# Kernel optimization log

Hardware: AMD Instinct MI355X
Metric: run time of the kernel (lower is better)

Reference implementation:

```python
import jax, jax.numpy as jnp
import numpy as np

N_SAMPLES = 16384
L = 8000   # num pseudo labels
C = 8      # num cameras
D = 256    # feature dim
N = 512    # batch size
T = 0.05   # temperature
K = 50     # hard_neg_k
LW = 0.5   # inter-cam loss weight


def setup_inputs() -> dict:
    key = jax.random.key(0)
    k1, k2, k3, k4, k5 = jax.random.split(key, 5)
    feats = jax.random.normal(k1, (N, D), dtype=jnp.float32)
    indexes = jax.random.randint(k2, (N,), 0, N_SAMPLES)
    label_table = jax.random.randint(k3, (N_SAMPLES,), 0, L)
    cam_table = jax.random.randint(k4, (N_SAMPLES,), 0, C)
    centers = jax.random.normal(k5, (L * C, D), dtype=jnp.float32)
    centers = centers / jnp.linalg.norm(centers, axis=1, keepdims=True)
    return {"feats": feats, "indexes": indexes, "label_table": label_table,
            "cam_table": cam_table, "centers": centers}


def reference(feats, indexes, label_table, cam_table, centers):
    # F.normalize(feats, p=2, dim=1)
    feats = feats / jnp.linalg.norm(feats, axis=1, keepdims=True)
    labels = label_table[indexes]          # [n]
    cams = cam_table[indexes]              # [n]
    cen = jax.lax.stop_gradient(centers)   # centers are a non-grad buffer in torch

    all_sims = feats @ cen.T               # [n, P]  P = L*C, proxy(l,c) = l*C + c
    n, P = all_sims.shape
    sims_r = all_sims.reshape(n, L, C)     # [n, L, C]

    # ---- intra-camera loss: softmax over the L proxies sharing sample's camera ----
    idx_cam = jnp.broadcast_to(cams[:, None, None], (n, L, 1))
    sims_intra = jnp.take_along_axis(sims_r, idx_cam, axis=2)[..., 0]  # [n, L]
    logp_intra = jax.nn.log_softmax(sims_intra / T, axis=1)
    loss_intra_i = -jnp.take_along_axis(logp_intra, labels[:, None], axis=1)[:, 0]

    # ---- inter-camera loss: C positives (same label, all cams) + top-K hard negatives ----
    idx_lab = jnp.broadcast_to(labels[:, None, None], (n, 1, C))
    pos_sims = jnp.take_along_axis(sims_r, idx_lab, axis=1)[:, 0, :]   # [n, C]
    masked = jnp.where(jnp.arange(L)[None, :, None] == labels[:, None, None],
                       jnp.float32(-10000.0), sims_r).reshape(n, P)
    neg_sims, _ = jax.lax.top_k(masked, K)                             # [n, K]
    logits = jnp.concatenate([pos_sims, neg_sims], axis=1) / T         # [n, C+K]
    logp = jax.nn.log_softmax(logits, axis=1)
    loss_inter_i = -jnp.mean(logp[:, :C], axis=1)  # target = 1/C on the C positives

    # ---- per-camera mean, summed over cameras (matches the torch.unique loop) ----
    ones = jnp.ones((n,), feats.dtype)
    counts = jax.ops.segment_sum(ones, cams, num_segments=C)
    safe = jnp.maximum(counts, 1.0)
    s_intra = jax.ops.segment_sum(loss_intra_i, cams, num_segments=C)
    s_inter = jax.ops.segment_sum(loss_inter_i, cams, num_segments=C)
    loss_intra = jnp.sum(jnp.where(counts > 0, s_intra / safe, 0.0))
    loss_inter = LW * jnp.sum(jnp.where(counts > 0, s_inter / safe, 0.0))
    return jnp.stack([loss_intra, loss_inter])
```

## Files before the change

### kernel.cpp

```cpp
#include <hip/hip_runtime.h>
#include <stdint.h>

#define NS   512
#define DDIM 256
#define LL   8000
#define CC   8
#define PP   64000
#define KTOP 50
#define CAP  1024
#define NBLK 2000
#define K2C  28.853900817779268f

typedef float f32x4 __attribute__((ext_vector_type(4)));
typedef short bf16x8 __attribute__((ext_vector_type(8)));

__device__ __forceinline__ ushort f2bf(float x) {
    uint32_t b = __float_as_uint(x);
    b += 0x7fffu + ((b >> 16) & 1u);
    return (ushort)(b >> 16);
}
__device__ __forceinline__ float bf2f(ushort u) {
    return __uint_as_float(((uint32_t)u) << 16);
}

__global__ void k_norm_gather(const float* __restrict__ feats,
                              const int* __restrict__ indexes,
                              const int* __restrict__ ltab,
                              const int* __restrict__ ctab,
                              ushort* __restrict__ feats_b,
                              int* __restrict__ labels,
                              int* __restrict__ cams) {
    const int n = blockIdx.x;
    const int lane = threadIdx.x;
    f32x4 v = ((const f32x4*)(feats + (size_t)n * DDIM))[lane];
    float ss = v[0]*v[0] + v[1]*v[1] + v[2]*v[2] + v[3]*v[3];
#pragma unroll
    for (int off = 32; off > 0; off >>= 1) ss += __shfl_down(ss, off);
    float tot = __shfl(ss, 0);
    float sc = 1.0f / sqrtf(tot);
    ushort4 o;
    o.x = f2bf(v[0] * sc); o.y = f2bf(v[1] * sc);
    o.z = f2bf(v[2] * sc); o.w = f2bf(v[3] * sc);
    ((ushort4*)(feats_b + (size_t)n * DDIM))[lane] = o;
    if (lane == 0) {
        int idx = indexes[n];
        labels[n] = ltab[idx];
        cams[n] = ctab[idx];
    }
}

__global__ __launch_bounds__(256) void k_sigma(const ushort* __restrict__ fb,
                                               const float* __restrict__ B,
                                               float* __restrict__ sig_acc) {
    __shared__ float cf[DDIM];
    __shared__ float red[256];
    const int tid = threadIdx.x;
    const int p = blockIdx.x * 997 + 123;
    cf[tid] = bf2f(f2bf(B[(size_t)p * DDIM + tid]));
    __syncthreads();
    float s = 0.0f;
#pragma unroll
    for (int rr = 0; rr < 2; ++rr) {
        int r = tid * 2 + rr;
        const ushort* a = fb + (size_t)r * DDIM;
        float d = 0.0f;
        for (int k = 0; k < DDIM; k += 8) {
            bf16x8 av = *(const bf16x8*)(a + k);
#pragma unroll
            for (int j = 0; j < 8; ++j) d += bf2f((ushort)av[j]) * cf[k + j];
        }
        s += d * d;
    }
    red[tid] = s;
    __syncthreads();
    for (int off = 128; off > 0; off >>= 1) {
        if (tid < off) red[tid] += red[tid + off];
        __syncthreads();
    }
    if (tid == 0) atomicAdd(sig_acc, red[0]);
}

__global__ __launch_bounds__(256, 4)
void k_gemm_fused(const ushort* __restrict__ A, const float* __restrict__ B,
                  const int* __restrict__ labels, const int* __restrict__ cams,
                  const float* __restrict__ sig_acc,
                  float* __restrict__ partial, float* __restrict__ cand,
                  int* __restrict__ gcount, float* __restrict__ posbuf) {
    const int bx   = blockIdx.x;
    const int cBase = bx * 32;
    const int tid  = threadIdx.x;
    const int lane = tid & 63;
    const int w    = tid >> 6;
    const int lr   = lane & 15;
    const int lk   = lane >> 4;

    __shared__ ushort sB[32][264];
    __shared__ int   s_lab[NS];
    __shared__ int   s_cam[NS];
    __shared__ float s_intra[NS];

#pragma unroll
    for (int it = 0; it < 8; ++it) {
        int q   = tid + it * 256;
        int col = q >> 6;
        int k4  = q & 63;
        f32x4 a = *(const f32x4*)(B + (size_t)(cBase + col) * DDIM + k4 * 4);
        ushort4 o;
        o.x = f2bf(a[0]); o.y = f2bf(a[1]); o.z = f2bf(a[2]); o.w = f2bf(a[3]);
        *(ushort4*)(&sB[col][k4 * 4]) = o;
    }
    for (int r = tid; r < NS; r += 256) {
        s_lab[r] = labels[r];
        s_cam[r] = cams[r];
        s_intra[r] = 0.0f;
    }
    __syncthreads();

    const float tau = 2.9f * sqrtf(sig_acc[0] * (1.0f / 32768.0f));

    f32x4 zero = {0.f, 0.f, 0.f, 0.f};
    f32x4 acc[8][2];
#pragma unroll
    for (int m = 0; m < 8; ++m) { acc[m][0] = zero; acc[m][1] = zero; }

#pragma unroll
    for (int kb = 0; kb < 8; ++kb) {
        const int kpos = kb * 32 + lk * 8;
        bf16x8 b0 = *(const bf16x8*)(&sB[lr][kpos]);
        bf16x8 b1 = *(const bf16x8*)(&sB[16 + lr][kpos]);
#pragma unroll
        for (int m = 0; m < 8; ++m) {
            bf16x8 a = *(const bf16x8*)(A + (size_t)(w * 128 + m * 16 + lr) * DDIM + kpos);
            acc[m][0] = __builtin_amdgcn_mfma_f32_16x16x32_bf16(a, b0, acc[m][0], 0, 0, 0);
            acc[m][1] = __builtin_amdgcn_mfma_f32_16x16x32_bf16(a, b1, acc[m][1], 0, 0, 0);
        }
    }

#pragma unroll
    for (int m = 0; m < 8; ++m) {
#pragma unroll
        for (int j = 0; j < 4; ++j) {
            const int r   = w * 128 + m * 16 + lk * 4 + j;
            const int lab = s_lab[r];
            const int cm  = s_cam[r];
#pragma unroll
            for (int nn = 0; nn < 2; ++nn) {
                const int c_loc = nn * 16 + lr;
                const float v = acc[m][nn][j];
                if ((c_loc & 7) == cm)
                    atomicAdd(&s_intra[r], exp2f(v * K2C));
                const int g = (cBase + c_loc) >> 3;
                if (g == lab) {
                    posbuf[r * CC + (c_loc & 7)] = v;
                } else if (v > tau) {
                    int id = atomicAdd(&gcount[r], 1);
                    if (id < CAP) cand[(size_t)r * CAP + id] = v;
                }
            }
        }
    }
    __syncthreads();
    for (int r = tid; r < NS; r += 256)
        partial[(size_t)bx * NS + r] = s_intra[r];
}

__global__ __launch_bounds__(256) void k_fixup(const ushort* __restrict__ fb,
                                               const float* __restrict__ B,
                                               const int* __restrict__ labels,
                                               float* __restrict__ cand,
                                               int* __restrict__ gcount) {
    const int n = blockIdx.x;
    const int c0 = gcount[n];
    if (c0 >= KTOP && c0 <= CAP) return;

    const int tid = threadIdx.x;
    __shared__ float f[DDIM];
    __shared__ float s_lo, s_hi;
    __shared__ int   red[256];
    __shared__ int   s_done;
    __shared__ int   s_cnt;
    if (tid < DDIM) f[tid] = bf2f(fb[(size_t)n * DDIM + tid]);
    const int label = labels[n];
    if (tid == 0) { s_lo = -1.01f; s_hi = 1.01f; s_done = 0; }
    __syncthreads();

    for (int it = 0; it < 16 && !s_done; ++it) {
        float tm = 0.5f * (s_lo + s_hi);
        int cnt = 0;
        for (int p = tid; p < PP; p += 256) {
            if ((p >> 3) == label) continue;
            const float* col = B + (size_t)p * DDIM;
            float d = 0.0f;
            for (int k = 0; k < DDIM; ++k) d += f[k] * bf2f(f2bf(col[k]));
            cnt += (d > tm);
        }
        red[tid] = cnt;
        __syncthreads();
        for (int off = 128; off > 0; off >>= 1) {
            if (tid < off) red[tid] += red[tid + off];
            __syncthreads();
        }
        int tot = red[0];
        __syncthreads();
        if (tot >= KTOP && tot <= CAP) {
            if (tid == 0) s_cnt = 0;
            __syncthreads();
            for (int p = tid; p < PP; p += 256) {
                if ((p >> 3) == label) continue;
                const float* col = B + (size_t)p * DDIM;
                float d = 0.0f;
                for (int k = 0; k < DDIM; ++k) d += f[k] * bf2f(f2bf(col[k]));
                if (d > tm) {
                    int id = atomicAdd(&s_cnt, 1);
                    if (id < CAP) cand[(size_t)n * CAP + id] = d;
                }
            }
            __syncthreads();
            if (tid == 0) { gcount[n] = (s_cnt > CAP) ? CAP : s_cnt; s_done = 1; }
            __syncthreads();
        } else {
            if (tid == 0) { if (tot < KTOP) s_hi = tm; else s_lo = tm; }
            __syncthreads();
        }
    }
    if (s_done) return;
    if (tid == 0) s_cnt = 0;
    __syncthreads();
    float tl = s_lo;
    for (int p = tid; p < PP; p += 256) {
        if ((p >> 3) == label) continue;
        const float* col = B + (size_t)p * DDIM;
        float d = 0.0f;
        for (int k = 0; k < DDIM; ++k) d += f[k] * bf2f(f2bf(col[k]));
        if (d > tl) {
            int id = atomicAdd(&s_cnt, 1);
            if (id < CAP) cand[(size_t)n * CAP + id] = d;
        }
    }
    __syncthreads();
    if (tid == 0) gcount[n] = (s_cnt > CAP) ? CAP : s_cnt;
}

__global__ __launch_bounds__(256) void k_row(const float* __restrict__ partial,
                                             const float* __restrict__ cand,
                                             const int* __restrict__ gcount,
                                             const float* __restrict__ posbuf,
                                             const int* __restrict__ labels,
                                             const int* __restrict__ cams,
                                             float* __restrict__ li,
                                             float* __restrict__ le) {
    const int n = blockIdx.x;
    const int tid = threadIdx.x;
    __shared__ float red[256];
    __shared__ float spos[CC];
    __shared__ float scand[CAP];

    float s = 0.0f;
    for (int b = tid; b < NBLK; b += 256) s += partial[(size_t)b * NS + n];
    red[tid] = s;
    __syncthreads();
    for (int off = 128; off > 0; off >>= 1) {
        if (tid < off) red[tid] += red[tid + off];
        __syncthreads();
    }
    if (tid < CC) spos[tid] = posbuf[n * CC + tid];
    __syncthreads();
    if (tid == 0) li[n] = logf(red[0]) * 0.6931471805599453f / 0.6931471805599453f - 20.0f * spos[cams[n]];
    __syncthreads();

    int c = gcount[n];
    if (c > CAP) c = CAP;
    for (int i = tid; i < c; i += 256) scand[i] = cand[(size_t)n * CAP + i];
    __syncthreads();
    float sum = 0.0f;
    for (int i = tid; i < c; i += 256) {
        float v = scand[i];
        int rk = 0;
        for (int j = 0; j < c; ++j) {
            float u = scand[j];
            rk += (u > v) || (u == v && j < i);
        }
        if (rk < KTOP) sum += exp2f(v * K2C);
    }
    if (tid < CC) sum += exp2f(spos[tid] * K2C);
    red[tid] = sum;
    __syncthreads();
    for (int off = 128; off > 0; off >>= 1) {
        if (tid < off) red[tid] += red[tid + off];
        __syncthreads();
    }
    if (tid == 0) {
        float ps = 0.0f;
#pragma unroll
        for (int j = 0; j < CC; ++j) ps += spos[j];
        le[n] = logf(red[0]) - 2.5f * ps;
    }
}

__global__ void k_finalize(const float* __restrict__ li, const float* __restrict__ le,
                           const int* __restrict__ cams, float* __restrict__ out) {
    __shared__ float si[CC], se[CC];
    __shared__ int sc[CC];
    int tid = threadIdx.x;
    if (tid < CC) { si[tid] = 0.f; se[tid] = 0.f; sc[tid] = 0; }
    __syncthreads();
    for (int i = tid; i < NS; i += 256) {
        int cm = cams[i];
        atomicAdd(&si[cm], li[i]);
        atomicAdd(&se[cm], le[i]);
        atomicAdd(&sc[cm], 1);
    }
    __syncthreads();
    if (tid == 0) {
        float a = 0.f, b = 0.f;
        for (int cm = 0; cm < CC; ++cm) {
            if (sc[cm] > 0) {
                a += si[cm] / (float)sc[cm];
                b += se[cm] / (float)sc[cm];
            }
        }
        out[0] = a;
        out[1] = 0.5f * b;
    }
}

extern "C" void kernel_launch(void* const* d_in, const int* in_sizes, int n_in,
                              void* d_out, int out_size, void* d_ws, size_t ws_size,
                              hipStream_t stream) {
    const float* feats   = (const float*)d_in[0];
    const int*   indexes = (const int*)d_in[1];
    const int*   ltab    = (const int*)d_in[2];
    const int*   ctab    = (const int*)d_in[3];
    const float* centers = (const float*)d_in[4];
    float* out = (float*)d_out;

    char* p = (char*)d_ws;
    float*  cand    = (float*)p;   p += (size_t)NS * CAP * sizeof(float);
    float*  partial = (float*)p;   p += (size_t)NBLK * NS * sizeof(float);
    float*  posbuf  = (float*)p;   p += (size_t)NS * CC * sizeof(float);
    ushort* fb      = (ushort*)p;  p += (size_t)NS * DDIM * sizeof(ushort);
    int*    labels  = (int*)p;     p += 2048;
    int*    cams    = (int*)p;     p += 2048;
    float*  li      = (float*)p;   p += 2048;
    float*  le      = (float*)p;   p += 2048;
    int*    gcount  = (int*)p;     p += 2048;
    float*  sig_acc = (float*)p;   p += 64;

    hipMemsetAsync(gcount, 0, 2048 + 64, stream);

    hipLaunchKernelGGL(k_norm_gather, dim3(NS), dim3(64), 0, stream,
                       feats, indexes, ltab, ctab, fb, labels, cams);
    hipLaunchKernelGGL(k_sigma, dim3(64), dim3(256), 0, stream,
                       fb, centers, sig_acc);
    hipLaunchKernelGGL(k_gemm_fused, dim3(NBLK), dim3(256), 0, stream,
                       fb, centers, labels, cams, sig_acc,
                       partial, cand, gcount, posbuf);
    hipLaunchKernelGGL(k_fixup, dim3(NS), dim3(256), 0, stream,
                       fb, centers, labels, cand, gcount);
    hipLaunchKernelGGL(k_row, dim3(NS), dim3(256), 0, stream,
                       partial, cand, gcount, posbuf, labels, cams, li, le);
    hipLaunchKernelGGL(k_finalize, dim3(1), dim3(256), 0, stream, li, le, cams, out);
}
```

Measured before the change: 235.5 us.

## Widen GEMM tiles, estimate threshold per block, fuse fixup into row kernel

Doubles the column tile of the fused GEMM to 64 proxies per block, which halves the block count and the partial-sum traffic, and prefetches the next A k-slice into registers. The separate sigma kernel is removed; each block now estimates its candidate threshold from its own accumulator values. The fixup fallback is merged into the row kernel, writing to shared memory instead of global. Clearing gcount moves into the gather kernel, replacing the memset, and intra sums are accumulated in registers before a single shared atomic. A per-block threshold can vary between blocks and make candidate selection less uniform, and the larger accumulator tile raises register pressure.

```diff
diff --git a/kernel.cpp b/kernel.cpp
--- a/kernel.cpp
+++ b/kernel.cpp
@@ -8,7 +8,8 @@
 #define PP   64000
 #define KTOP 50
 #define CAP  1024
-#define NBLK 2000
+#define BC   64
+#define NBLK (PP/BC)
 #define K2C  28.853900817779268f
 
 typedef float f32x4 __attribute__((ext_vector_type(4)));
@@ -29,7 +30,8 @@
                               const int* __restrict__ ctab,
                               ushort* __restrict__ feats_b,
                               int* __restrict__ labels,
-                              int* __restrict__ cams) {
+                              int* __restrict__ cams,
+                              int* __restrict__ gcount) {
     const int n = blockIdx.x;
     const int lane = threadIdx.x;
     f32x4 v = ((const f32x4*)(feats + (size_t)n * DDIM))[lane];
@@ -46,61 +48,34 @@
         int idx = indexes[n];
         labels[n] = ltab[idx];
         cams[n] = ctab[idx];
-    }
-}
-
-__global__ __launch_bounds__(256) void k_sigma(const ushort* __restrict__ fb,
-                                               const float* __restrict__ B,
-                                               float* __restrict__ sig_acc) {
-    __shared__ float cf[DDIM];
-    __shared__ float red[256];
-    const int tid = threadIdx.x;
-    const int p = blockIdx.x * 997 + 123;
-    cf[tid] = bf2f(f2bf(B[(size_t)p * DDIM + tid]));
-    __syncthreads();
-    float s = 0.0f;
-#pragma unroll
-    for (int rr = 0; rr < 2; ++rr) {
-        int r = tid * 2 + rr;
-        const ushort* a = fb + (size_t)r * DDIM;
-        float d = 0.0f;
-        for (int k = 0; k < DDIM; k += 8) {
-            bf16x8 av = *(const bf16x8*)(a + k);
-#pragma unroll
-            for (int j = 0; j < 8; ++j) d += bf2f((ushort)av[j]) * cf[k + j];
-        }
-        s += d * d;
-    }
-    red[tid] = s;
-    __syncthreads();
-    for (int off = 128; off > 0; off >>= 1) {
-        if (tid < off) red[tid] += red[tid + off];
-        __syncthreads();
-    }
-    if (tid == 0) atomicAdd(sig_acc, red[0]);
-}
-
-__global__ __launch_bounds__(256, 4)
+        gcount[n] = 0;
+    }
+}
+
+__global__ __launch_bounds__(256, 2)
 void k_gemm_fused(const ushort* __restrict__ A, const float* __restrict__ B,
                   const int* __restrict__ labels, const int* __restrict__ cams,
-                  const float* __restrict__ sig_acc,
                   float* __restrict__ partial, float* __restrict__ cand,
                   int* __restrict__ gcount, float* __restrict__ posbuf) {
-    const int bx   = blockIdx.x;
-    const int cBase = bx * 32;
-    const int tid  = threadIdx.x;
-    const int lane = tid & 63;
-    const int w    = tid >> 6;
-    const int lr   = lane & 15;
-    const int lk   = lane >> 4;
-
-    __shared__ ushort sB[32][264];
-    __shared__ int   s_lab[NS];
-    __shared__ int   s_cam[NS];
-    __shared__ float s_intra[NS];
-
-#pragma unroll
-    for (int it = 0; it < 8; ++it) {
+    const int bx    = blockIdx.x;
+    const int cBase = bx * BC;
+    const int gBase = cBase >> 3;
+    const int tid   = threadIdx.x;
+    const int lane  = tid & 63;
+    const int w     = tid >> 6;
+    const int lr    = lane & 15;
+    const int lk    = lane >> 4;
+
+    __shared__ ushort sB[BC][264];
+    __shared__ int    s_lab[NS];
+    __shared__ int    s_cam[NS];
+    __shared__ float  s_intra[NS];
+    __shared__ float  s_redA[256];
+    __shared__ float  s_redB[256];
+    __shared__ float  s_tau;
+
+#pragma unroll
+    for (int it = 0; it < 16; ++it) {
         int q   = tid + it * 256;
         int col = q >> 6;
         int k4  = q & 63;
@@ -116,25 +91,62 @@
     }
     __syncthreads();
 
-    const float tau = 2.9f * sqrtf(sig_acc[0] * (1.0f / 32768.0f));
+    const ushort* Abase = A + (size_t)(w * 128) * DDIM;
+    bf16x8 acur[8];
+#pragma unroll
+    for (int m = 0; m < 8; ++m)
+        acur[m] = *(const bf16x8*)(Abase + (size_t)(m * 16 + lr) * DDIM + lk * 8);
 
     f32x4 zero = {0.f, 0.f, 0.f, 0.f};
-    f32x4 acc[8][2];
-#pragma unroll
-    for (int m = 0; m < 8; ++m) { acc[m][0] = zero; acc[m][1] = zero; }
+    f32x4 acc[8][4];
+#pragma unroll
+    for (int m = 0; m < 8; ++m)
+#pragma unroll
+        for (int nn = 0; nn < 4; ++nn) acc[m][nn] = zero;
 
 #pragma unroll
     for (int kb = 0; kb < 8; ++kb) {
         const int kpos = kb * 32 + lk * 8;
-        bf16x8 b0 = *(const bf16x8*)(&sB[lr][kpos]);
-        bf16x8 b1 = *(const bf16x8*)(&sB[16 + lr][kpos]);
-#pragma unroll
-        for (int m = 0; m < 8; ++m) {
-            bf16x8 a = *(const bf16x8*)(A + (size_t)(w * 128 + m * 16 + lr) * DDIM + kpos);
-            acc[m][0] = __builtin_amdgcn_mfma_f32_16x16x32_bf16(a, b0, acc[m][0], 0, 0, 0);
-            acc[m][1] = __builtin_amdgcn_mfma_f32_16x16x32_bf16(a, b1, acc[m][1], 0, 0, 0);
-        }
-    }
+        bf16x8 bfr[4];
+#pragma unroll
+        for (int nn = 0; nn < 4; ++nn)
+            bfr[nn] = *(const bf16x8*)(&sB[nn * 16 + lr][kpos]);
+        bf16x8 anxt[8];
+        if (kb < 7) {
+#pragma unroll
+            for (int m = 0; m < 8; ++m)
+                anxt[m] = *(const bf16x8*)(Abase + (size_t)(m * 16 + lr) * DDIM + kpos + 32);
+        }
+#pragma unroll
+        for (int m = 0; m < 8; ++m)
+#pragma unroll
+            for (int nn = 0; nn < 4; ++nn)
+                acc[m][nn] = __builtin_amdgcn_mfma_f32_16x16x32_bf16(acur[m], bfr[nn], acc[m][nn], 0, 0, 0);
+        if (kb < 7) {
+#pragma unroll
+            for (int m = 0; m < 8; ++m) acur[m] = anxt[m];
+        }
+    }
+
+    float ss = 0.0f, sc2 = 0.0f;
+#pragma unroll
+    for (int m = 0; m < 8; ++m)
+#pragma unroll
+        for (int nn = 0; nn < 4; ++nn)
+#pragma unroll
+            for (int j = 0; j < 4; ++j) {
+                float v = acc[m][nn][j];
+                if (fabsf(v) < 0.25f) { ss += v * v; sc2 += 1.0f; }
+            }
+    s_redA[tid] = ss; s_redB[tid] = sc2;
+    __syncthreads();
+    for (int off = 128; off > 0; off >>= 1) {
+        if (tid < off) { s_redA[tid] += s_redA[tid + off]; s_redB[tid] += s_redB[tid + off]; }
+        __syncthreads();
+    }
+    if (tid == 0) s_tau = 2.9f * sqrtf(s_redA[0] / fmaxf(s_redB[0], 1.0f));
+    __syncthreads();
+    const float tau = s_tau;
 
 #pragma unroll
     for (int m = 0; m < 8; ++m) {
@@ -143,20 +155,22 @@
             const int r   = w * 128 + m * 16 + lk * 4 + j;
             const int lab = s_lab[r];
             const int cm  = s_cam[r];
-#pragma unroll
-            for (int nn = 0; nn < 2; ++nn) {
-                const int c_loc = nn * 16 + lr;
+            const bool mycam  = ((lr & 7) == cm);
+            const bool hasLab = ((unsigned)(lab - gBase) < 8u);
+            float isum = 0.0f;
+#pragma unroll
+            for (int nn = 0; nn < 4; ++nn) {
                 const float v = acc[m][nn][j];
-                if ((c_loc & 7) == cm)
-                    atomicAdd(&s_intra[r], exp2f(v * K2C));
-                const int g = (cBase + c_loc) >> 3;
-                if (g == lab) {
-                    posbuf[r * CC + (c_loc & 7)] = v;
+                if (mycam) isum += exp2f(v * K2C);
+                const int g = gBase + ((nn * 16 + lr) >> 3);
+                if (hasLab && g == lab) {
+                    posbuf[r * CC + (lr & 7)] = v;
                 } else if (v > tau) {
                     int id = atomicAdd(&gcount[r], 1);
                     if (id < CAP) cand[(size_t)r * CAP + id] = v;
                 }
             }
+            if (mycam) atomicAdd(&s_intra[r], isum);
         }
     }
     __syncthreads();
@@ -164,114 +178,102 @@
         partial[(size_t)bx * NS + r] = s_intra[r];
 }
 
-__global__ __launch_bounds__(256) void k_fixup(const ushort* __restrict__ fb,
-                                               const float* __restrict__ B,
-                                               const int* __restrict__ labels,
-                                               float* __restrict__ cand,
-                                               int* __restrict__ gcount) {
+__global__ __launch_bounds__(256)
+void k_row(const ushort* __restrict__ fb, const float* __restrict__ B,
+           const float* __restrict__ partial, const float* __restrict__ cand,
+           const int* __restrict__ gcount, const float* __restrict__ posbuf,
+           const int* __restrict__ labels, const int* __restrict__ cams,
+           float* __restrict__ li, float* __restrict__ le) {
     const int n = blockIdx.x;
-    const int c0 = gcount[n];
-    if (c0 >= KTOP && c0 <= CAP) return;
-
     const int tid = threadIdx.x;
+    __shared__ float red[256];
+    __shared__ int   redi[256];
+    __shared__ float spos[CC];
+    __shared__ float scand[CAP];
     __shared__ float f[DDIM];
     __shared__ float s_lo, s_hi;
-    __shared__ int   red[256];
-    __shared__ int   s_done;
-    __shared__ int   s_cnt;
-    if (tid < DDIM) f[tid] = bf2f(fb[(size_t)n * DDIM + tid]);
-    const int label = labels[n];
-    if (tid == 0) { s_lo = -1.01f; s_hi = 1.01f; s_done = 0; }
-    __syncthreads();
-
-    for (int it = 0; it < 16 && !s_done; ++it) {
-        float tm = 0.5f * (s_lo + s_hi);
-        int cnt = 0;
-        for (int p = tid; p < PP; p += 256) {
-            if ((p >> 3) == label) continue;
-            const float* col = B + (size_t)p * DDIM;
-            float d = 0.0f;
-            for (int k = 0; k < DDIM; ++k) d += f[k] * bf2f(f2bf(col[k]));
-            cnt += (d > tm);
-        }
-        red[tid] = cnt;
-        __syncthreads();
-        for (int off = 128; off > 0; off >>= 1) {
-            if (tid < off) red[tid] += red[tid + off];
-            __syncthreads();
-        }
-        int tot = red[0];
-        __syncthreads();
-        if (tot >= KTOP && tot <= CAP) {
-            if (tid == 0) s_cnt = 0;
-            __syncthreads();
+    __shared__ int   s_done, s_cnt;
+
+    float s = 0.0f;
+    for (int b = tid; b < NBLK; b += 256) s += partial[(size_t)b * NS + n];
+    red[tid] = s;
+    __syncthreads();
+    for (int off = 128; off > 0; off >>= 1) {
+        if (tid < off) red[tid] += red[tid + off];
+        __syncthreads();
+    }
+    if (tid < CC) spos[tid] = posbuf[n * CC + tid];
+    __syncthreads();
+    if (tid == 0) li[n] = logf(red[0]) - 20.0f * spos[cams[n]];
+
+    int c = gcount[n];
+    if (c >= KTOP && c <= CAP) {
+        for (int i = tid; i < c; i += 256) scand[i] = cand[(size_t)n * CAP + i];
+    } else {
+        if (tid < DDIM) f[tid] = bf2f(fb[(size_t)n * DDIM + tid]);
+        const int label = labels[n];
+        if (tid == 0) { s_lo = -1.01f; s_hi = 1.01f; s_done = 0; s_cnt = 0; }
+        __syncthreads();
+        for (int it = 0; it < 16; ++it) {
+            if (s_done) break;
+            float tm = 0.5f * (s_lo + s_hi);
+            int cnt = 0;
             for (int p = tid; p < PP; p += 256) {
                 if ((p >> 3) == label) continue;
                 const float* col = B + (size_t)p * DDIM;
                 float d = 0.0f;
                 for (int k = 0; k < DDIM; ++k) d += f[k] * bf2f(f2bf(col[k]));
-                if (d > tm) {
+                cnt += (d > tm);
+            }
+            redi[tid] = cnt;
+            __syncthreads();
+            for (int off = 128; off > 0; off >>= 1) {
+                if (tid < off) redi[tid] += redi[tid + off];
+                __syncthreads();
+            }
+            int tot = redi[0];
+            __syncthreads();
+            if (tot >= KTOP && tot <= CAP) {
+                if (tid == 0) s_cnt = 0;
+                __syncthreads();
+                for (int p = tid; p < PP; p += 256) {
+                    if ((p >> 3) == label) continue;
+                    const float* col = B + (size_t)p * DDIM;
+                    float d = 0.0f;
+                    for (int k = 0; k < DDIM; ++k) d += f[k] * bf2f(f2bf(col[k]));
+                    if (d > tm) {
+                        int id = atomicAdd(&s_cnt, 1);
+                        if (id < CAP) scand[id] = d;
+                    }
+                }
+                __syncthreads();
+                if (tid == 0) s_done = 1;
+            } else {
+                if (tid == 0) { if (tot < KTOP) s_hi = tm; else s_lo = tm; }
+            }
+            __syncthreads();
+        }
+        if (!s_done) {
+            if (tid == 0) s_cnt = 0;
+            __syncthreads();
+            float tl = s_lo;
+            for (int p = tid; p < PP; p += 256) {
+                if ((p >> 3) == label) continue;
+                const float* col = B + (size_t)p * DDIM;
+                float d = 0.0f;
+                for (int k = 0; k < DDIM; ++k) d += f[k] * bf2f(f2bf(col[k]));
+                if (d > tl) {
                     int id = atomicAdd(&s_cnt, 1);
-                    if (id < CAP) cand[(size_t)n * CAP + id] = d;
+                    if (id < CAP) scand[id] = d;
                 }
             }
-            __syncthreads();
-            if (tid == 0) { gcount[n] = (s_cnt > CAP) ? CAP : s_cnt; s_done = 1; }
-            __syncthreads();
-        } else {
-            if (tid == 0) { if (tot < KTOP) s_hi = tm; else s_lo = tm; }
-            __syncthreads();
-        }
-    }
-    if (s_done) return;
-    if (tid == 0) s_cnt = 0;
-    __syncthreads();
-    float tl = s_lo;
-    for (int p = tid; p < PP; p += 256) {
-        if ((p >> 3) == label) continue;
-        const float* col = B + (size_t)p * DDIM;
-        float d = 0.0f;
-        for (int k = 0; k < DDIM; ++k) d += f[k] * bf2f(f2bf(col[k]));
-        if (d > tl) {
-            int id = atomicAdd(&s_cnt, 1);
-            if (id < CAP) cand[(size_t)n * CAP + id] = d;
-        }
-    }
-    __syncthreads();
-    if (tid == 0) gcount[n] = (s_cnt > CAP) ? CAP : s_cnt;
-}
-
-__global__ __launch_bounds__(256) void k_row(const float* __restrict__ partial,
-                                             const float* __restrict__ cand,
-                                             const int* __restrict__ gcount,
-                                             const float* __restrict__ posbuf,
-                                             const int* __restrict__ labels,
-                                             const int* __restrict__ cams,
-                                             float* __restrict__ li,
-                                             float* __restrict__ le) {
-    const int n = blockIdx.x;
-    const int tid = threadIdx.x;
-    __shared__ float red[256];
-    __shared__ float spos[CC];
-    __shared__ float scand[CAP];
-
-    float s = 0.0f;
-    for (int b = tid; b < NBLK; b += 256) s += partial[(size_t)b * NS + n];
-    red[tid] = s;
-    __syncthreads();
-    for (int off = 128; off > 0; off >>= 1) {
-        if (tid < off) red[tid] += red[tid + off];
-        __syncthreads();
-    }
-    if (tid < CC) spos[tid] = posbuf[n * CC + tid];
-    __syncthreads();
-    if (tid == 0) li[n] = logf(red[0]) * 0.6931471805599453f / 0.6931471805599453f - 20.0f * spos[cams[n]];
-    __syncthreads();
-
-    int c = gcount[n];
-    if (c > CAP) c = CAP;
-    for (int i = tid; i < c; i += 256) scand[i] = cand[(size_t)n * CAP + i];
-    __syncthreads();
+        }
+        __syncthreads();
+        c = s_cnt;
+        if (c > CAP) c = CAP;
+    }
+    __syncthreads();
+
     float sum = 0.0f;
     for (int i = tid; i < c; i += 256) {
         float v = scand[i];
@@ -344,20 +346,12 @@
     float*  li      = (float*)p;   p += 2048;
     float*  le      = (float*)p;   p += 2048;
     int*    gcount  = (int*)p;     p += 2048;
-    float*  sig_acc = (float*)p;   p += 64;
-
-    hipMemsetAsync(gcount, 0, 2048 + 64, stream);
 
     hipLaunchKernelGGL(k_norm_gather, dim3(NS), dim3(64), 0, stream,
-                       feats, indexes, ltab, ctab, fb, labels, cams);
-    hipLaunchKernelGGL(k_sigma, dim3(64), dim3(256), 0, stream,
-                       fb, centers, sig_acc);
+                       feats, indexes, ltab, ctab, fb, labels, cams, gcount);
     hipLaunchKernelGGL(k_gemm_fused, dim3(NBLK), dim3(256), 0, stream,
-                       fb, centers, labels, cams, sig_acc,
-                       partial, cand, gcount, posbuf);
-    hipLaunchKernelGGL(k_fixup, dim3(NS), dim3(256), 0, stream,
-                       fb, centers, labels, cand, gcount);
+                       fb, centers, labels, cams, partial, cand, gcount, posbuf);
     hipLaunchKernelGGL(k_row, dim3(NS), dim3(256), 0, stream,
-                       partial, cand, gcount, posbuf, labels, cams, li, le);
+                       fb, centers, partial, cand, gcount, posbuf, labels, cams, li, le);
     hipLaunchKernelGGL(k_finalize, dim3(1), dim3(256), 0, stream, li, le, cams, out);
 }
```

Result: faster. 218.3 us (-7.3%).
